# Performance work log

Measured on AMD Instinct MI355X. Metric: run time of the kernel, lower is better.

The kernel has to match this reference:

```python
import jax, jax.numpy as jnp
import numpy as np

N_NODES = 65536
N_PER = 1024      # nodes per graph
NUM_GRAPHS = 64
N_EDGES = 1048576
IN_DIM = 192
PE_DIM = 64
HIDDEN = 256
LATENT = 128
POOL_RATIO = 0.5
K_PER = int(np.ceil(POOL_RATIO * N_PER))  # 512 kept per graph


def setup_inputs() -> dict:
    key = jax.random.key(0)
    ks = jax.random.split(key, 12)
    x_raw = jax.random.normal(ks[0], (N_NODES, IN_DIM), dtype=jnp.float32)
    sincos_pe = jax.random.normal(ks[1], (N_NODES, PE_DIM), dtype=jnp.float32)
    edge_index = jax.random.randint(ks[2], (2, N_EDGES), 0, N_NODES, dtype=jnp.int64)
    batch = (jnp.arange(N_NODES, dtype=jnp.int64) // N_PER)
    eps = jax.random.normal(ks[3], (N_NODES, LATENT), dtype=jnp.float32)
    # learned parameters (GCNConv: Linear no-bias weight + separate bias; TopKPooling weight)
    def glorot(k, shape):
        lim = float(np.sqrt(6.0 / (shape[0] + shape[1])))
        return jax.random.uniform(k, shape, jnp.float32, -lim, lim)
    W1 = glorot(ks[4], (IN_DIM + PE_DIM, HIDDEN))
    b1 = jnp.zeros((HIDDEN,), jnp.float32)
    Wmu = glorot(ks[5], (HIDDEN, LATENT))
    bmu = jnp.zeros((LATENT,), jnp.float32)
    Wlv = glorot(ks[6], (HIDDEN, LATENT))
    blv = jnp.zeros((LATENT,), jnp.float32)
    w_pool = jax.random.uniform(ks[7], (LATENT,), jnp.float32, -1.0, 1.0) / np.sqrt(LATENT)
    return {"x_raw": x_raw, "sincos_pe": sincos_pe, "edge_index": edge_index,
            "batch": batch, "eps": eps, "W1": W1, "b1": b1, "Wmu": Wmu,
            "bmu": bmu, "Wlv": Wlv, "blv": blv, "w_pool": w_pool}


def _gcn_conv(x, W, b, src, dst, n):
    # PyG GCNConv: x' = D^{-1/2}(A+I)D^{-1/2} (x W) + b, self-loops already in src/dst
    h = x @ W                                   # [N, out]
    deg = jnp.zeros((n,), h.dtype).at[dst].add(1.0)
    dinv = jax.lax.rsqrt(deg)                   # deg >= 1 thanks to self-loops
    norm = dinv[src] * dinv[dst]                # [E+N]
    msg = norm[:, None] * h[src]                # gather (irregular)
    return jax.ops.segment_sum(msg, dst, num_segments=n) + b


def reference(x_raw, sincos_pe, edge_index, batch, eps, W1, b1, Wmu, bmu, Wlv, blv, w_pool):
    n = x_raw.shape[0]
    loops = jnp.arange(n, dtype=edge_index.dtype)
    src = jnp.concatenate([edge_index[0], loops])
    dst = jnp.concatenate([edge_index[1], loops])

    x_in = jnp.concatenate([x_raw, sincos_pe], axis=-1)
    h = jax.nn.relu(_gcn_conv(x_in, W1, b1, src, dst, n))
    mu = _gcn_conv(h, Wmu, bmu, src, dst, n)
    logvar = _gcn_conv(h, Wlv, blv, src, dst, n)
    z = mu + eps * jnp.exp(0.5 * logvar)

    # TopKPooling: score = tanh((z . w)/||w||); keep top ratio per graph
    score = jnp.tanh((z @ w_pool) / jnp.linalg.norm(w_pool))   # [N]
    s2 = score.reshape(NUM_GRAPHS, N_PER)
    _, idx = jax.lax.top_k(s2, K_PER)                           # descending per graph
    perm = (idx + (jnp.arange(NUM_GRAPHS) * N_PER)[:, None]).reshape(-1)
    z_pool = z[perm] * score[perm][:, None]
    mu_pool = mu[perm]
    logvar_pool = logvar[perm]
    batch_pool = batch[perm]
    return z_pool, mu_pool, logvar_pool, batch_pool, perm
```

## Files before the change

### kernel.cpp

```cpp
#include <hip/hip_runtime.h>
#include <hip/hip_fp16.h>
#include <math.h>

#define NN      65536
#define NE      1048576
#define NPER    1024
#define NGRAPH  64
#define KPER    512
#define IND     192
#define PED     64
#define HID     256
#define LAT     128

#define OFF_CNT     0u
#define OFF_ROWPTR  65536u
#define OFF_CUR     132096u
#define OFF_DINV    198656u
#define OFF_EPK     264192u
#define OFF_INVWN   2361344u
#define OFF_KEEP    2361360u
#define OFF_SCORE   2395136u
#define OFF_WT1     2460672u
#define OFF_WT2     2493440u
#define OFF_T0B     2526208u
#define OFF_HB      6720512u
#define OFF_MUB     6720512u
#define OFF_LVB     10914816u

#define OUT_MU      4194304
#define OUT_LV      8388608
#define OUT_BATCH   12582912
#define OUT_PERM    12615680

typedef __attribute__((ext_vector_type(8))) short short8;
typedef __attribute__((ext_vector_type(4))) float floatx4;

__device__ __forceinline__ unsigned short f2bf(float f) {
    unsigned int u = __float_as_uint(f);
    u += 0x7FFFu + ((u >> 16) & 1u);
    return (unsigned short)(u >> 16);
}
__device__ __forceinline__ float bf2f(unsigned short u) {
    return __uint_as_float(((unsigned int)u) << 16);
}
__device__ __forceinline__ unsigned int pack2bf(float x, float y) {
    const unsigned int ux = __float_as_uint(x) + 0x8000u;
    const unsigned int uy = __float_as_uint(y) + 0x8000u;
    return __builtin_amdgcn_perm(uy, ux, 0x07060302u);
}
__device__ __forceinline__ unsigned char f2e5(float f) {
    unsigned short u = __half_as_ushort(__float2half(f));
    u += (unsigned short)(0x7Fu + ((u >> 8) & 1u));
    return (unsigned char)(u >> 8);
}
__device__ __forceinline__ unsigned int pack4e5(float v0, float v1, float v2, float v3) {
#if __has_builtin(__builtin_amdgcn_cvt_pk_bf8_f32)
    const int t0 = __builtin_amdgcn_cvt_pk_bf8_f32(v0, v1, 0, false);
    return (unsigned int)__builtin_amdgcn_cvt_pk_bf8_f32(v2, v3, t0, true);
#else
    return (unsigned int)f2e5(v0) | ((unsigned int)f2e5(v1) << 8) |
           ((unsigned int)f2e5(v2) << 16) | ((unsigned int)f2e5(v3) << 24);
#endif
}
__device__ __forceinline__ __half2 e5lo(unsigned int u) {
    return __builtin_bit_cast(__half2, __builtin_amdgcn_perm(u, 0u, 0x05000400u));
}
__device__ __forceinline__ __half2 e5hi(unsigned int u) {
    return __builtin_bit_cast(__half2, __builtin_amdgcn_perm(u, 0u, 0x07000600u));
}
__device__ __forceinline__ __half2 meta2w(unsigned int m) {
    return __builtin_bit_cast(__half2, __builtin_amdgcn_perm(m, m, 0x07060706u));
}

__global__ __launch_bounds__(256) void k_count(const int* __restrict__ ei, int* __restrict__ cnt) {
    const int g = blockIdx.x * 256 + threadIdx.x;
    const int4 d4 = *(const int4*)(ei + NE + g * 4);
    atomicAdd(&cnt[d4.x], 1);
    atomicAdd(&cnt[d4.y], 1);
    atomicAdd(&cnt[d4.z], 1);
    atomicAdd(&cnt[d4.w], 1);
}

__global__ __launch_bounds__(256) void k_scanA(const int* __restrict__ cnt, int* __restrict__ rp,
                                               float* __restrict__ dinv, int* __restrict__ bsum) {
    __shared__ int sh[256];
    const int t = threadIdx.x, b = blockIdx.x;
    const int i = b * 256 + t;
    const int c = cnt[i];
    sh[t] = c;
    __syncthreads();
    for (int d = 1; d < 256; d <<= 1) {
        const int v = (t >= d) ? sh[t - d] : 0;
        __syncthreads();
        sh[t] += v;
        __syncthreads();
    }
    rp[i] = sh[t] - c;
    dinv[i] = 1.0f / sqrtf((float)(c + 1));
    if (t == 255) bsum[b] = sh[t];
}

__global__ __launch_bounds__(256) void k_scanB(int* __restrict__ bsum) {
    __shared__ int sh[256];
    const int t = threadIdx.x;
    const int c = bsum[t];
    sh[t] = c;
    __syncthreads();
    for (int d = 1; d < 256; d <<= 1) {
        const int v = (t >= d) ? sh[t - d] : 0;
        __syncthreads();
        sh[t] += v;
        __syncthreads();
    }
    bsum[t] = sh[t] - c;
}

__global__ __launch_bounds__(256) void k_scanC(int* __restrict__ rp, const int* __restrict__ bsum) {
    const int t = threadIdx.x, b = blockIdx.x;
    const int i = b * 256 + t;
    rp[i] += bsum[b];
    if (i == NN - 1) rp[NN] = NE;
}

__global__ __launch_bounds__(256) void k_scatter(const int* __restrict__ ei, const int* __restrict__ rp,
                                                 int* __restrict__ cur, const float* __restrict__ dinv,
                                                 unsigned int* __restrict__ epk) {
    int e = blockIdx.x * 256 + threadIdx.x;
    int s = ei[e];
    int d = ei[NE + e];
    int pos = rp[d] + atomicAdd(&cur[d], 1);
    const unsigned short hn = __half_as_ushort(__float2half(dinv[s] * dinv[d]));
    epk[pos] = ((unsigned int)hn << 16) | (unsigned int)s;
}

__global__ __launch_bounds__(128) void k_wnorm(const float* __restrict__ wp, float* __restrict__ invwn) {
    __shared__ float red[128];
    int t = threadIdx.x;
    float v = wp[t];
    red[t] = v * v;
    __syncthreads();
    for (int s = 64; s > 0; s >>= 1) {
        if (t < s) red[t] += red[t + s];
        __syncthreads();
    }
    if (t == 0) invwn[0] = 1.0f / sqrtf(red[0]);
}

__global__ __launch_bounds__(256) void k_prepw(const float* __restrict__ W1, const float* __restrict__ Wmu,
                                               const float* __restrict__ Wlv, unsigned short* __restrict__ wt1,
                                               unsigned short* __restrict__ wt2) {
    const int n = blockIdx.x, k = threadIdx.x;
    wt1[n * 256 + k] = f2bf(W1[k * 256 + n]);
    wt2[n * 256 + k] = f2bf((n < 128) ? Wmu[k * 128 + n] : Wlv[k * 128 + (n - 128)]);
}

template <int MODE>
__global__ __launch_bounds__(256, 2) void k_gemm(const float* __restrict__ A0f, const float* __restrict__ A1f,
                                                 const unsigned short* __restrict__ Ah,
                                                 const unsigned short* __restrict__ Wt,
                                                 unsigned char* __restrict__ Cb) {
    __shared__ unsigned short lds[2][12288];
    const int tid = threadIdx.x;
    const int w = __builtin_amdgcn_readfirstlane(tid >> 6);
    const int lane = tid & 63;
    const int l = lane & 15, q = lane >> 4;
    const int Rbase = blockIdx.x * 128;
    const int mtb = (w >> 1) * 4;
    const int ntb = (w & 1) * 8;

    const int rs = tid >> 1;
    const int ch = tid & 1;
    const int stile = rs >> 4, sl = rs & 15, q0 = ch * 2;
    const int uA = (stile * 4 + q0) * 16 + sl;

    floatx4 acc[8][4];
#pragma unroll
    for (int j = 0; j < 8; ++j)
#pragma unroll
        for (int m = 0; m < 4; ++m) acc[j][m] = (floatx4)0.0f;

    auto stage = [&](int ks, int buf) {
        if (MODE == 0) {
            const float* p; int ld, col;
            const int k = ks * 32 + ch * 16;
            if (ks < 6) { p = A0f; ld = IND; col = k; }
            else        { p = A1f; ld = PED; col = k - IND; }
            const float* src = p + (size_t)(Rbase + rs) * ld + col;
            unsigned int pk[8];
#pragma unroll
            for (int j = 0; j < 16; j += 4) {
                const float4 t = *(const float4*)(src + j);
                pk[j / 2]     = pack2bf(t.x, t.y);
                pk[j / 2 + 1] = pack2bf(t.z, t.w);
            }
            *(uint4*)&lds[buf][uA * 8]        = *(uint4*)&pk[0];
            *(uint4*)&lds[buf][(uA + 16) * 8] = *(uint4*)&pk[4];
        } else {
            const unsigned short* src = Ah + (size_t)(Rbase + rs) * 256 + ks * 32 + ch * 16;
            *(uint4*)&lds[buf][uA * 8]        = ((const uint4*)src)[0];
            *(uint4*)&lds[buf][(uA + 16) * 8] = ((const uint4*)src)[1];
        }
#pragma unroll
        for (int rep = 0; rep < 2; ++rep) {
            const int n = rep * 128 + rs;
            const unsigned short* srcB = Wt + (size_t)n * 256 + ks * 32 + ch * 16;
            const uint4 w0 = ((const uint4*)srcB)[0];
            const uint4 w1 = ((const uint4*)srcB)[1];
            const int uB = ((n >> 4) * 4 + q0) * 16 + (n & 15);
            *(uint4*)&lds[buf][4096 + uB * 8]        = w0;
            *(uint4*)&lds[buf][4096 + (uB + 16) * 8] = w1;
        }
    };

    stage(0, 0);
    __syncthreads();
#pragma unroll
    for (int ks = 0; ks < 8; ++ks) {
        const int cur = ks & 1;
        if (ks < 7) stage(ks + 1, cur ^ 1);
        short8 a[4];
#pragma unroll
        for (int m = 0; m < 4; ++m)
            a[m] = *(const short8*)&lds[cur][(((mtb + m) * 4 + q) * 16 + l) * 8];
#pragma unroll
        for (int j = 0; j < 8; ++j) {
            const short8 b = *(const short8*)&lds[cur][4096 + (((ntb + j) * 4 + q) * 16 + l) * 8];
#pragma unroll
            for (int m = 0; m < 4; ++m)
                acc[j][m] = __builtin_amdgcn_mfma_f32_16x16x32_bf16(b, a[m], acc[j][m], 0, 0, 0);
        }
        if (ks < 7) __syncthreads();
    }

#pragma unroll
    for (int m = 0; m < 4; ++m) {
        const int row = Rbase + (mtb + m) * 16 + l;
#pragma unroll
        for (int j = 0; j < 8; ++j) {
            const int col = (ntb + j) * 16 + q * 4;
            const floatx4 v = acc[j][m];
            *(unsigned int*)(Cb + ((size_t)(col >> 5) * NN + row) * 32 + (col & 31)) =
                pack4e5(v[0], v[1], v[2], v[3]);
        }
    }
}

template <int PHASE>
__global__ __launch_bounds__(256) void k_agg(const unsigned char* __restrict__ tb, const int* __restrict__ rp,
                                             const unsigned int* __restrict__ epk, const float* __restrict__ dinv,
                                             const float* __restrict__ bias0, const float* __restrict__ bias1,
                                             const float* __restrict__ eps, const float* __restrict__ wp,
                                             unsigned short* __restrict__ hb, unsigned short* __restrict__ mub,
                                             unsigned short* __restrict__ lvb, float* __restrict__ score) {
    const int lane = threadIdx.x & 63;
    const int slice = blockIdx.x & 7;
    const int node = (blockIdx.x >> 3) * 32 + (threadIdx.x >> 6) * 8 + (lane >> 3);
    const int lo4 = (lane & 7) * 4;
    const unsigned char* tsl = tb + ((size_t)slice * NN) * 32 + lo4;

    const float di = dinv[node];
    const unsigned int vs = *(const unsigned int*)(tsl + ((size_t)node << 5));
    const __half2 ws2 = __float2half2_rn(di * di);
    __half2 a01 = __hmul2(ws2, e5lo(vs));
    __half2 a23 = __hmul2(ws2, e5hi(vs));
    __half2 b01 = __float2half2_rn(0.0f);
    __half2 b23 = __float2half2_rn(0.0f);

    int p = rp[node];
    const int end = rp[node + 1];
    unsigned int m0 = epk[p], m1 = epk[p + 1];
    unsigned int v0 = *(const unsigned int*)(tsl + ((size_t)(m0 & 0xFFFFu) << 5));
    unsigned int v1 = *(const unsigned int*)(tsl + ((size_t)(m1 & 0xFFFFu) << 5));
    while (p + 2 <= end) {
        const unsigned int n0 = epk[p + 2], n1 = epk[p + 3];
        const unsigned int u0 = *(const unsigned int*)(tsl + ((size_t)(n0 & 0xFFFFu) << 5));
        const unsigned int u1 = *(const unsigned int*)(tsl + ((size_t)(n1 & 0xFFFFu) << 5));
        const __half2 w0 = meta2w(m0);
        const __half2 w1 = meta2w(m1);
        a01 = __hfma2(w0, e5lo(v0), a01); a23 = __hfma2(w0, e5hi(v0), a23);
        b01 = __hfma2(w1, e5lo(v1), b01); b23 = __hfma2(w1, e5hi(v1), b23);
        m0 = n0; m1 = n1; v0 = u0; v1 = u1; p += 2;
    }
    if (p < end) {
        const __half2 w0 = meta2w(m0);
        a01 = __hfma2(w0, e5lo(v0), a01);
        a23 = __hfma2(w0, e5hi(v0), a23);
    }
    a01 = __hadd2(a01, b01);
    a23 = __hadd2(a23, b23);
    const float2 flo = __half22float2(a01);
    const float2 fhi = __half22float2(a23);
    float4 acc = make_float4(flo.x, flo.y, fhi.x, fhi.y);
    const int c = slice * 32 + lo4;

    if (PHASE == 0) {
        const float4 bb = *(const float4*)(bias0 + c);
        ushort4 r;
        r.x = f2bf(fmaxf(acc.x + bb.x, 0.0f));
        r.y = f2bf(fmaxf(acc.y + bb.y, 0.0f));
        r.z = f2bf(fmaxf(acc.z + bb.z, 0.0f));
        r.w = f2bf(fmaxf(acc.w + bb.w, 0.0f));
        *(ushort4*)(hb + (size_t)node * 256 + c) = r;
    } else {
        float partial;
        if (c < 128) {
            const float4 bb = *(const float4*)(bias0 + c);
            acc.x += bb.x; acc.y += bb.y; acc.z += bb.z; acc.w += bb.w;
            ushort4 st;
            st.x = f2bf(acc.x); st.y = f2bf(acc.y); st.z = f2bf(acc.z); st.w = f2bf(acc.w);
            *(ushort4*)(mub + (size_t)node * 128 + c) = st;
            const float4 w4 = *(const float4*)(wp + c);
            partial = acc.x * w4.x + acc.y * w4.y + acc.z * w4.z + acc.w * w4.w;
        } else {
            const int cl = c - 128;
            const float4 bb = *(const float4*)(bias1 + cl);
            acc.x += bb.x; acc.y += bb.y; acc.z += bb.z; acc.w += bb.w;
            ushort4 st;
            st.x = f2bf(acc.x); st.y = f2bf(acc.y); st.z = f2bf(acc.z); st.w = f2bf(acc.w);
            *(ushort4*)(lvb + (size_t)node * 128 + cl) = st;
            const float4 w4 = *(const float4*)(wp + cl);
            const float4 e4 = *(const float4*)(eps + (size_t)node * 128 + cl);
            partial = e4.x * expf(0.5f * acc.x) * w4.x + e4.y * expf(0.5f * acc.y) * w4.y +
                      e4.z * expf(0.5f * acc.z) * w4.z + e4.w * expf(0.5f * acc.w) * w4.w;
        }
        partial += __shfl_xor(partial, 1, 64);
        partial += __shfl_xor(partial, 2, 64);
        partial += __shfl_xor(partial, 4, 64);
        if ((lane & 7) == 0) atomicAdd(&score[node], partial);
    }
}

__global__ __launch_bounds__(512) void k_topk(const float* __restrict__ score, const int* __restrict__ batch,
                                              int* __restrict__ keep, float* __restrict__ out) {
    __shared__ float sk[1024];
    __shared__ int si[1024];
    const int g = blockIdx.x, t = threadIdx.x;
    for (int i = t; i < 1024; i += 512) {
        sk[i] = score[g * 1024 + i];
        si[i] = i;
    }
    __syncthreads();
    for (int k = 2; k <= 1024; k <<= 1) {
        for (int j = k >> 1; j > 0; j >>= 1) {
            for (int base = 0; base < 1024; base += 512) {
                int i = base + t;
                int ixj = i ^ j;
                if (ixj > i) {
                    float a = sk[i], b = sk[ixj];
                    int ia = si[i], ib = si[ixj];
                    bool before = (a > b) || (a == b && ia < ib);
                    bool up = ((i & k) == 0);
                    bool sw = up ? (!before) : before;
                    if (sw) {
                        sk[i] = b; si[i] = ib;
                        sk[ixj] = a; si[ixj] = ia;
                    }
                }
            }
            __syncthreads();
        }
    }
    if (t < KPER) {
        int node = g * 1024 + si[t];
        keep[g * KPER + t] = node;
        out[OUT_BATCH + g * KPER + t] = (float)batch[node];
        out[OUT_PERM + g * KPER + t] = (float)node;
    }
}

__global__ __launch_bounds__(128) void k_gather(const int* __restrict__ keep,
                                                const unsigned short* __restrict__ mub,
                                                const unsigned short* __restrict__ lvb,
                                                const float* __restrict__ eps,
                                                const float* __restrict__ score,
                                                const float* __restrict__ invwn, float* __restrict__ out) {
    const int kidx = blockIdx.x;
    const int c = threadIdx.x;
    const int node = keep[kidx];
    const float m = bf2f(mub[(size_t)node * 128 + c]);
    const float l = bf2f(lvb[(size_t)node * 128 + c]);
    const float e = eps[(size_t)node * 128 + c];
    const float z = fmaf(e, expf(0.5f * l), m);
    const float s = tanhf(score[node] * invwn[0]);
    out[(size_t)kidx * 128 + c] = z * s;
    out[OUT_MU + (size_t)kidx * 128 + c] = m;
    out[OUT_LV + (size_t)kidx * 128 + c] = l;
}

extern "C" void kernel_launch(void* const* d_in, const int* in_sizes, int n_in,
                              void* d_out, int out_size, void* d_ws, size_t ws_size,
                              hipStream_t stream) {
    (void)in_sizes; (void)n_in; (void)out_size; (void)ws_size;
    const float* x_raw = (const float*)d_in[0];
    const float* pe    = (const float*)d_in[1];
    const int*   ei    = (const int*)d_in[2];
    const int*   batch = (const int*)d_in[3];
    const float* eps   = (const float*)d_in[4];
    const float* W1    = (const float*)d_in[5];
    const float* b1    = (const float*)d_in[6];
    const float* Wmu   = (const float*)d_in[7];
    const float* bmu   = (const float*)d_in[8];
    const float* Wlv   = (const float*)d_in[9];
    const float* blv   = (const float*)d_in[10];
    const float* wp    = (const float*)d_in[11];
    float* ws = (float*)d_ws;
    int*  iws = (int*)d_ws;
    unsigned int* epk = (unsigned int*)(iws + OFF_EPK);
    unsigned short* wt1  = (unsigned short*)(ws + OFF_WT1);
    unsigned short* wt2  = (unsigned short*)(ws + OFF_WT2);
    unsigned char*  t0b  = (unsigned char*)(ws + OFF_T0B);
    unsigned short* hb16 = (unsigned short*)(ws + OFF_HB);
    unsigned short* mub  = (unsigned short*)(ws + OFF_MUB);
    unsigned short* lvb  = (unsigned short*)(ws + OFF_LVB);
    float* out = (float*)d_out;

    hipMemsetAsync(iws + OFF_CNT, 0, 65536 * 4, stream);
    hipMemsetAsync(iws + OFF_CUR, 0, 65536 * 4, stream);
    hipMemsetAsync(ws + OFF_SCORE, 0, 65536 * 4, stream);

    k_count<<<NE / 1024, 256, 0, stream>>>(ei, iws + OFF_CNT);
    k_scanA<<<256, 256, 0, stream>>>(iws + OFF_CNT, iws + OFF_ROWPTR, ws + OFF_DINV, iws + OFF_KEEP);
    k_scanB<<<1, 256, 0, stream>>>(iws + OFF_KEEP);
    k_scanC<<<256, 256, 0, stream>>>(iws + OFF_ROWPTR, iws + OFF_KEEP);
    k_scatter<<<NE / 256, 256, 0, stream>>>(ei, iws + OFF_ROWPTR, iws + OFF_CUR, ws + OFF_DINV, epk);
    k_wnorm<<<1, 128, 0, stream>>>(wp, ws + OFF_INVWN);
    k_prepw<<<256, 256, 0, stream>>>(W1, Wmu, Wlv, wt1, wt2);

    k_gemm<0><<<NN / 128, 256, 0, stream>>>(x_raw, pe, nullptr, wt1, t0b);
    k_agg<0><<<(NN / 32) * 8, 256, 0, stream>>>(t0b, iws + OFF_ROWPTR, epk, ws + OFF_DINV,
                                                b1, nullptr, nullptr, nullptr,
                                                hb16, nullptr, nullptr, nullptr);
    k_gemm<1><<<NN / 128, 256, 0, stream>>>(nullptr, nullptr, hb16, wt2, t0b);
    k_agg<1><<<(NN / 32) * 8, 256, 0, stream>>>(t0b, iws + OFF_ROWPTR, epk, ws + OFF_DINV,
                                                bmu, blv, eps, wp,
                                                nullptr, mub, lvb, ws + OFF_SCORE);
    k_topk<<<NGRAPH, 512, 0, stream>>>(ws + OFF_SCORE, batch, iws + OFF_KEEP, out);
    k_gather<<<NGRAPH * KPER, 128, 0, stream>>>(iws + OFF_KEEP, mub, lvb, eps,
                                                ws + OFF_SCORE, ws + OFF_INVWN, out);
}
```

Measured before the change: 493.5 us.

## Spread each node's edges across 8 lane groups with shuffle reduction in aggregation

The GCN aggregation kernel changes from one 8-lane group per node walking that node's edge list serially to a wavefront that processes 8 consecutive nodes in turn. For each node, the 8 edge-lanes take strided edges from the CSR range and the partial sums are combined with cross-lane half2 shuffles. The aim is to even out load imbalance across nodes of different degree and keep more gathers in flight through a 3-deep prefetch. In exchange it adds shuffle reductions, masked wasted lanes at node boundaries, and only one lane group doing the epilogue.

```diff
diff --git a/kernel.cpp b/kernel.cpp
--- a/kernel.cpp
+++ b/kernel.cpp
@@ -71,6 +71,9 @@
 __device__ __forceinline__ __half2 meta2w(unsigned int m) {
     return __builtin_bit_cast(__half2, __builtin_amdgcn_perm(m, m, 0x07060706u));
 }
+__device__ __forceinline__ __half2 shflx_h2(__half2 x, int m) {
+    return __builtin_bit_cast(__half2, __shfl_xor(__builtin_bit_cast(int, x), m, 64));
+}
 
 __global__ __launch_bounds__(256) void k_count(const int* __restrict__ ei, int* __restrict__ cnt) {
     const int g = blockIdx.x * 256 + threadIdx.x;
@@ -252,81 +255,99 @@
                                              const float* __restrict__ eps, const float* __restrict__ wp,
                                              unsigned short* __restrict__ hb, unsigned short* __restrict__ mub,
                                              unsigned short* __restrict__ lvb, float* __restrict__ score) {
-    const int lane = threadIdx.x & 63;
+    const int tid = threadIdx.x;
+    const int lane = tid & 63;
+    const int e = lane >> 3;
+    const int c = lane & 7;
     const int slice = blockIdx.x & 7;
-    const int node = (blockIdx.x >> 3) * 32 + (threadIdx.x >> 6) * 8 + (lane >> 3);
-    const int lo4 = (lane & 7) * 4;
-    const unsigned char* tsl = tb + ((size_t)slice * NN) * 32 + lo4;
-
-    const float di = dinv[node];
-    const unsigned int vs = *(const unsigned int*)(tsl + ((size_t)node << 5));
-    const __half2 ws2 = __float2half2_rn(di * di);
-    __half2 a01 = __hmul2(ws2, e5lo(vs));
-    __half2 a23 = __hmul2(ws2, e5hi(vs));
-    __half2 b01 = __float2half2_rn(0.0f);
-    __half2 b23 = __float2half2_rn(0.0f);
-
-    int p = rp[node];
-    const int end = rp[node + 1];
-    unsigned int m0 = epk[p], m1 = epk[p + 1];
+    const int nbase = (blockIdx.x >> 3) * 32 + (tid >> 6) * 8;
+    const unsigned char* tsl = tb + ((size_t)slice * NN) * 32 + c * 4;
+    const int ccol = slice * 32 + c * 4;
+    const bool isLv = (PHASE == 1) && (slice >= 4);
+
+    float4 bb, w4;
+    if (PHASE == 0) {
+        bb = *(const float4*)(bias0 + ccol);
+    } else if (!isLv) {
+        bb = *(const float4*)(bias0 + ccol);
+        w4 = *(const float4*)(wp + ccol);
+    } else {
+        bb = *(const float4*)(bias1 + (ccol - 128));
+        w4 = *(const float4*)(wp + (ccol - 128));
+    }
+
+    int b = rp[nbase];
+    int be = b + e;
+    unsigned int m0 = epk[be], m1 = epk[be + 8], m2 = epk[be + 16];
     unsigned int v0 = *(const unsigned int*)(tsl + ((size_t)(m0 & 0xFFFFu) << 5));
     unsigned int v1 = *(const unsigned int*)(tsl + ((size_t)(m1 & 0xFFFFu) << 5));
-    while (p + 2 <= end) {
-        const unsigned int n0 = epk[p + 2], n1 = epk[p + 3];
-        const unsigned int u0 = *(const unsigned int*)(tsl + ((size_t)(n0 & 0xFFFFu) << 5));
-        const unsigned int u1 = *(const unsigned int*)(tsl + ((size_t)(n1 & 0xFFFFu) << 5));
-        const __half2 w0 = meta2w(m0);
-        const __half2 w1 = meta2w(m1);
-        a01 = __hfma2(w0, e5lo(v0), a01); a23 = __hfma2(w0, e5hi(v0), a23);
-        b01 = __hfma2(w1, e5lo(v1), b01); b23 = __hfma2(w1, e5hi(v1), b23);
-        m0 = n0; m1 = n1; v0 = u0; v1 = u1; p += 2;
-    }
-    if (p < end) {
-        const __half2 w0 = meta2w(m0);
-        a01 = __hfma2(w0, e5lo(v0), a01);
-        a23 = __hfma2(w0, e5hi(v0), a23);
-    }
-    a01 = __hadd2(a01, b01);
-    a23 = __hadd2(a23, b23);
-    const float2 flo = __half22float2(a01);
-    const float2 fhi = __half22float2(a23);
-    float4 acc = make_float4(flo.x, flo.y, fhi.x, fhi.y);
-    const int c = slice * 32 + lo4;
-
-    if (PHASE == 0) {
-        const float4 bb = *(const float4*)(bias0 + c);
-        ushort4 r;
-        r.x = f2bf(fmaxf(acc.x + bb.x, 0.0f));
-        r.y = f2bf(fmaxf(acc.y + bb.y, 0.0f));
-        r.z = f2bf(fmaxf(acc.z + bb.z, 0.0f));
-        r.w = f2bf(fmaxf(acc.w + bb.w, 0.0f));
-        *(ushort4*)(hb + (size_t)node * 256 + c) = r;
-    } else {
-        float partial;
-        if (c < 128) {
-            const float4 bb = *(const float4*)(bias0 + c);
-            acc.x += bb.x; acc.y += bb.y; acc.z += bb.z; acc.w += bb.w;
-            ushort4 st;
-            st.x = f2bf(acc.x); st.y = f2bf(acc.y); st.z = f2bf(acc.z); st.w = f2bf(acc.w);
-            *(ushort4*)(mub + (size_t)node * 128 + c) = st;
-            const float4 w4 = *(const float4*)(wp + c);
-            partial = acc.x * w4.x + acc.y * w4.y + acc.z * w4.z + acc.w * w4.w;
-        } else {
-            const int cl = c - 128;
-            const float4 bb = *(const float4*)(bias1 + cl);
-            acc.x += bb.x; acc.y += bb.y; acc.z += bb.z; acc.w += bb.w;
-            ushort4 st;
-            st.x = f2bf(acc.x); st.y = f2bf(acc.y); st.z = f2bf(acc.z); st.w = f2bf(acc.w);
-            *(ushort4*)(lvb + (size_t)node * 128 + cl) = st;
-            const float4 w4 = *(const float4*)(wp + cl);
-            const float4 e4 = *(const float4*)(eps + (size_t)node * 128 + cl);
-            partial = e4.x * expf(0.5f * acc.x) * w4.x + e4.y * expf(0.5f * acc.y) * w4.y +
-                      e4.z * expf(0.5f * acc.z) * w4.z + e4.w * expf(0.5f * acc.w) * w4.w;
-        }
-        partial += __shfl_xor(partial, 1, 64);
-        partial += __shfl_xor(partial, 2, 64);
-        partial += __shfl_xor(partial, 4, 64);
-        if ((lane & 7) == 0) atomicAdd(&score[node], partial);
+    unsigned int v2 = *(const unsigned int*)(tsl + ((size_t)(m2 & 0xFFFFu) << 5));
+
+    int hi = b;
+    for (int ni = 0; ni < 8; ++ni) {
+        const int node = nbase + ni;
+        const int lo = hi;
+        hi = rp[node + 1];
+        const float di = dinv[node];
+        const unsigned int vs = *(const unsigned int*)(tsl + ((size_t)node << 5));
+        float4 e4;
+        if (isLv) e4 = *(const float4*)(eps + (size_t)node * 128 + (ccol - 128));
+
+        const __half2 hz = __float2half2_rn(0.0f);
+        __half2 a01 = hz, a23 = hz;
+        for (;;) {
+            const bool val = (be >= lo) && (be < hi);
+            __half2 w = meta2w(m0);
+            w = val ? w : hz;
+            a01 = __hfma2(w, e5lo(v0), a01);
+            a23 = __hfma2(w, e5hi(v0), a23);
+            if (b + 8 > hi) break;
+            m0 = m1; v0 = v1; m1 = m2; v1 = v2;
+            b += 8; be += 8;
+            m2 = epk[be + 16];
+            v2 = *(const unsigned int*)(tsl + ((size_t)(m2 & 0xFFFFu) << 5));
+        }
+        a01 = __hadd2(a01, shflx_h2(a01, 8));
+        a01 = __hadd2(a01, shflx_h2(a01, 16));
+        a01 = __hadd2(a01, shflx_h2(a01, 32));
+        a23 = __hadd2(a23, shflx_h2(a23, 8));
+        a23 = __hadd2(a23, shflx_h2(a23, 16));
+        a23 = __hadd2(a23, shflx_h2(a23, 32));
+        if (e == 0) {
+            const float2 flo = __half22float2(a01);
+            const float2 fhi = __half22float2(a23);
+            const float2 slo = __half22float2(e5lo(vs));
+            const float2 shi = __half22float2(e5hi(vs));
+            const float d2 = di * di;
+            const float ax = fmaf(d2, slo.x, flo.x) + bb.x;
+            const float ay = fmaf(d2, slo.y, flo.y) + bb.y;
+            const float az = fmaf(d2, shi.x, fhi.x) + bb.z;
+            const float aw = fmaf(d2, shi.y, fhi.y) + bb.w;
+            if (PHASE == 0) {
+                ushort4 r;
+                r.x = f2bf(fmaxf(ax, 0.0f));
+                r.y = f2bf(fmaxf(ay, 0.0f));
+                r.z = f2bf(fmaxf(az, 0.0f));
+                r.w = f2bf(fmaxf(aw, 0.0f));
+                *(ushort4*)(hb + (size_t)node * 256 + ccol) = r;
+            } else {
+                ushort4 st;
+                st.x = f2bf(ax); st.y = f2bf(ay); st.z = f2bf(az); st.w = f2bf(aw);
+                float partial;
+                if (!isLv) {
+                    *(ushort4*)(mub + (size_t)node * 128 + ccol) = st;
+                    partial = ax * w4.x + ay * w4.y + az * w4.z + aw * w4.w;
+                } else {
+                    *(ushort4*)(lvb + (size_t)node * 128 + (ccol - 128)) = st;
+                    partial = e4.x * expf(0.5f * ax) * w4.x + e4.y * expf(0.5f * ay) * w4.y +
+                              e4.z * expf(0.5f * az) * w4.z + e4.w * expf(0.5f * aw) * w4.w;
+                }
+                partial += __shfl_xor(partial, 1, 64);
+                partial += __shfl_xor(partial, 2, 64);
+                partial += __shfl_xor(partial, 4, 64);
+                if (c == 0) atomicAdd(&score[node], partial);
+            }
+        }
     }
 }
 
```

New measurement: 670.8 us. 35.9% more time.
